# Performance work log

Measured on AMD Instinct MI355X. Metric: run time of the kernel, lower is better.

Reference implementation:

```python
import jax, jax.numpy as jnp
import numpy as np

# ----- constants derived from SNNNetwork.__init__ kwargs -----
T, B = 500, 32                     # steps = sim_time/dt = 25/0.05
ARCH = [512, 1024, 512]
DT = 0.05
R = 1.0 / 9.43
I0 = 700.0
K_M = 1.0 / (R * I0 * DT)          # as in __init__: k_m = 1/(R*I0*dt)
THRESH = 10.0                      # fixed plausible threshold (torch code derives it from `target`, but is non-runnable)
SPIKE_R = 20.0
SIGMA_V = 10.0
V_RESET = 0.0
ASC_AMP = np.array([-9.18, -198.94], np.float32)
ASC_R = np.array([1.0, 1.0], np.float32)
ASC_K = np.array([0.003, 0.1], np.float32)


def setup_inputs() -> dict:
    key = jax.random.key(0)
    k1, k2, k3 = jax.random.split(key, 3)
    inputs = jax.random.normal(k1, (T, B, ARCH[0]), dtype=jnp.float32)
    # nn.init.uniform_(linear.weight, wt-1, wt+1); use small symmetric range
    W1 = jax.random.uniform(k2, (ARCH[1], ARCH[0]), jnp.float32, -0.05, 0.05)
    W2 = jax.random.uniform(k3, (ARCH[2], ARCH[1]), jnp.float32, -0.05, 0.05)
    return {"inputs": inputs, "W1": W1, "W2": W2}


def _neuron_step(state, x):
    """One GLIFR (rate-based GLIF with after-spike currents) update.
    state = (v [B,N], asc [2,B,N]); x is synaptic drive [B,N].
    Returns (new_state, spikes [B,N]).
    """
    v, asc = state
    amp = jnp.asarray(ASC_AMP)[:, None, None]
    rmul = jnp.asarray(ASC_R)[:, None, None]
    kasc = jnp.asarray(ASC_K)[:, None, None]
    syn = I0 * x                                          # k_syn = 1
    i_total = syn + asc.sum(0)
    s = SPIKE_R * jax.nn.sigmoid((v - THRESH) / SIGMA_V)  # smooth spike rate
    s_dt = s * DT
    asc_new = asc * (1.0 - DT * kasc) + s_dt * (rmul * asc + amp)
    v_new = v + DT * K_M * (R * i_total - (v - V_RESET)) + s_dt * (V_RESET - v)
    return (v_new, asc_new), s


def reference(inputs, W1, W2):
    Bc = inputs.shape[1]

    def zstate(n):
        return (jnp.zeros((Bc, n), inputs.dtype), jnp.zeros((2, Bc, n), inputs.dtype))

    init = (zstate(ARCH[0]), jnp.zeros((Bc, ARCH[0]), inputs.dtype),
            zstate(ARCH[1]), jnp.zeros((Bc, ARCH[1]), inputs.dtype),
            zstate(ARCH[2]))

    def step(carry, x):
        st0, buf0, st1, buf1, st2 = carry
        # layer 0: no linear, raw input drives the neuron
        st0, s0 = _neuron_step(st0, x)
        # layer 1: delayed (delay=1) spikes of layer 0 through Linear
        st1, s1 = _neuron_step(st1, buf0 @ W1.T)
        # layer 2: delayed spikes of layer 1 through Linear
        st2, s2 = _neuron_step(st2, buf1 @ W2.T)
        return (st0, s0, st1, s1, st2), s2

    _, spikes_all = jax.lax.scan(step, init, inputs)
    return spikes_all  # [T, B, ARCH[-1]] == layers[-1].spikes_all
```

## Files before the change

kernel.cpp:

```cpp
#include <hip/hip_runtime.h>
#include <hip/hip_bf16.h>
#include <stdint.h>

#define TSTEPS 500
#define BB 32
#define N0 512
#define N1 1024
#define N2 512

typedef unsigned short ushort_t;
typedef __attribute__((ext_vector_type(8))) short short8;
typedef __attribute__((ext_vector_type(4))) float f32x4;

__device__ __forceinline__ ushort_t f2b(float x) {
    union { float f; uint32_t u; } c; c.f = x;
    uint32_t r = (c.u + 0x7fffu + ((c.u >> 16) & 1u)) >> 16;
    return (ushort_t)r;
}
__device__ __forceinline__ float b2f(ushort_t u) {
    union { uint32_t u; float f; } c; c.u = ((uint32_t)u) << 16;
    return c.f;
}

__device__ __forceinline__ float glifr_step(float& v, float& a0, float& a1,
                                            float x) {
    const float INV_I0 = 1.0f / 700.0f;
    const float C2 = 9.43f / 700.0f;
    const float CE = 0.14426950408889634f;
    const float CE10 = 1.4426950408889634f;
    const float C0 = 1.0f - 0.05f * 0.003f;
    const float C1 = 1.0f - 0.05f * 0.1f;
    const float AMP0 = -9.18f, AMP1 = -198.94f;

    float asum = a0 + a1;
    float drv = fmaf(asum, INV_I0, x);
    float e = exp2f(fmaf(v, -CE, CE10));
    float sig = __builtin_amdgcn_rcpf(1.0f + e);
    float na0 = fmaf(sig, a0 + AMP0, a0 * C0);
    float na1 = fmaf(sig, a1 + AMP1, a1 * C1);
    float nv = fmaf(-sig, v, fmaf(-C2, v, v + drv));
    a0 = na0; a1 = na1; v = nv;
    return sig;
}

#define PD 20
template <int NW, int MODE>
__global__ void scan_kernel(const float* __restrict__ drive,
                            float* __restrict__ sout) {
    const int idx = blockIdx.x * blockDim.x + threadIdx.x;
    const int S = BB * NW;

    auto LD = [&](int t) -> float {
        if (MODE == 0) return drive[(size_t)t * S + idx];
        return (t == 0) ? 0.0f : drive[(size_t)(t - 1) * S + idx];
    };

    float v = 0.f, a0 = 0.f, a1 = 0.f;

    auto STEP = [&](int t, float x) {
        float sig = glifr_step(v, a0, a1, x);
        sout[(size_t)t * S + idx] = (MODE == 2) ? 20.0f * sig : sig;
    };

    float p[PD];
#pragma unroll
    for (int i = 0; i < PD; ++i) p[i] = LD(i);

    for (int t = 0; t < TSTEPS - PD; t += PD) {
        float q[PD];
#pragma unroll
        for (int i = 0; i < PD; ++i) q[i] = LD(t + PD + i);
#pragma unroll
        for (int i = 0; i < PD; ++i) STEP(t + i, p[i]);
#pragma unroll
        for (int i = 0; i < PD; ++i) p[i] = q[i];
    }
#pragma unroll
    for (int i = 0; i < PD; ++i) STEP(TSTEPS - PD + i, p[i]);
}

__global__ void wsplit(const float* __restrict__ W1, const float* __restrict__ W2,
                       ushort_t* __restrict__ w1h, ushort_t* __restrict__ w1l,
                       ushort_t* __restrict__ w2h, ushort_t* __restrict__ w2l) {
    int i = blockIdx.x * 256 + threadIdx.x;
    float a = 20.0f * W1[i];
    ushort_t h = f2b(a);
    w1h[i] = h; w1l[i] = f2b(a - b2f(h));
    float b = 20.0f * W2[i];
    h = f2b(b);
    w2h[i] = h; w2l[i] = f2b(b - b2f(h));
}

template <int NBY>
__global__ __launch_bounds__(256, 2) void gemm_x3(
    const float* __restrict__ A,
    const ushort_t* __restrict__ Bh, const ushort_t* __restrict__ Bl,
    float* __restrict__ C, int Ncols, int K) {
    __shared__ char lds[32768];
    const int tid = threadIdx.x;
    const int lane = tid & 63, wave = tid >> 6;

    const int id = blockIdx.x, nwg = gridDim.x;
    const int qq = nwg >> 3, rr = nwg & 7;
    const int xcd = id & 7, jj = id >> 3;
    const int wg = (xcd < rr ? xcd * (qq + 1) : rr * (qq + 1) + (xcd - rr) * qq) + jj;
    const int m0 = (wg / NBY) * 128;
    const int n0 = (wg % NBY) * 128;

    const ushort_t* gB = (wave == 2) ? Bh : Bl;
    const int chunk_sw = (lane & 3) ^ ((lane >> 3) & 3);
    const size_t rowbB = (size_t)K * 2;
    const char* gsrcB = (const char*)gB +
                        (size_t)(n0 + (lane >> 2)) * rowbB + (size_t)chunk_sw * 16;

    const int r0 = tid >> 3, c4 = tid & 7;
    const int ch = (c4 >> 1) ^ ((r0 >> 1) & 3);
    const int aoff = r0 * 64 + ch * 16 + (c4 & 1) * 8;
    const float* aSrc = A + (size_t)(m0 + r0) * K + c4 * 4;

    const int KSTEPS = K / 32;
    f32x4 acc[4][4];
#pragma unroll
    for (int i = 0; i < 4; ++i)
#pragma unroll
        for (int j = 0; j < 4; ++j) acc[i][j] = (f32x4){0.f, 0.f, 0.f, 0.f};

    const int wm = wave >> 1, wn = wave & 1;
    const int r4 = lane & 15, kg = lane >> 4;
    const int slot = kg ^ ((r4 >> 1) & 3);
    const int fA = (wm * 64 + r4) * 64 + slot * 16;
    const int fB = (wn * 64 + r4) * 64 + slot * 16;

    for (int ks = 0; ks < KSTEPS; ++ks) {
        if (wave >= 2) {
#pragma unroll
            for (int i = 0; i < 8; ++i) {
                __builtin_amdgcn_global_load_lds(
                    (const __attribute__((address_space(1))) uint32_t*)(
                        gsrcB + (size_t)i * 16 * rowbB + (size_t)ks * 64),
                    (__attribute__((address_space(3))) uint32_t*)(
                        lds + 16384 + (wave - 2) * 8192 + i * 1024),
                    16, 0, 0);
            }
        }
#pragma unroll
        for (int i = 0; i < 4; ++i) {
            const float4 av = *reinterpret_cast<const float4*>(
                aSrc + (size_t)i * 32 * K + (size_t)ks * 32);
            __hip_bfloat162 h01 = __float22bfloat162_rn(make_float2(av.x, av.y));
            __hip_bfloat162 h23 = __float22bfloat162_rn(make_float2(av.z, av.w));
            uint32_t hi01 = *reinterpret_cast<uint32_t*>(&h01);
            uint32_t hi23 = *reinterpret_cast<uint32_t*>(&h23);
            float lx = av.x - __uint_as_float(hi01 << 16);
            float ly = av.y - __uint_as_float(hi01 & 0xffff0000u);
            float lz = av.z - __uint_as_float(hi23 << 16);
            float lw = av.w - __uint_as_float(hi23 & 0xffff0000u);
            __hip_bfloat162 l01 = __float22bfloat162_rn(make_float2(lx, ly));
            __hip_bfloat162 l23 = __float22bfloat162_rn(make_float2(lz, lw));
            uint32_t lo01 = *reinterpret_cast<uint32_t*>(&l01);
            uint32_t lo23 = *reinterpret_cast<uint32_t*>(&l23);
            *reinterpret_cast<uint2*>(lds + aoff + i * 2048) =
                make_uint2(hi01, hi23);
            *reinterpret_cast<uint2*>(lds + 8192 + aoff + i * 2048) =
                make_uint2(lo01, lo23);
        }
        __syncthreads();

        short8 ah[4], al[4], bh[4], bl[4];
#pragma unroll
        for (int i = 0; i < 4; ++i) {
            ah[i] = *(const short8*)(lds + 0     + fA + i * 1024);
            al[i] = *(const short8*)(lds + 8192  + fA + i * 1024);
            bh[i] = *(const short8*)(lds + 16384 + fB + i * 1024);
            bl[i] = *(const short8*)(lds + 24576 + fB + i * 1024);
        }
#pragma unroll
        for (int i = 0; i < 4; ++i)
#pragma unroll
            for (int j = 0; j < 4; ++j) {
                acc[i][j] = __builtin_amdgcn_mfma_f32_16x16x32_bf16(
                    ah[i], bh[j], acc[i][j], 0, 0, 0);
                acc[i][j] = __builtin_amdgcn_mfma_f32_16x16x32_bf16(
                    ah[i], bl[j], acc[i][j], 0, 0, 0);
                acc[i][j] = __builtin_amdgcn_mfma_f32_16x16x32_bf16(
                    al[i], bh[j], acc[i][j], 0, 0, 0);
            }
        __syncthreads();
    }

#pragma unroll
    for (int i = 0; i < 4; ++i)
#pragma unroll
        for (int j = 0; j < 4; ++j)
#pragma unroll
            for (int r = 0; r < 4; ++r) {
                int row = m0 + wm * 64 + i * 16 + kg * 4 + r;
                int col = n0 + wn * 64 + j * 16 + r4;
                C[(size_t)row * Ncols + col] = acc[i][j][r];
            }
}

extern "C" void kernel_launch(void* const* d_in, const int* in_sizes, int n_in,
                              void* d_out, int out_size, void* d_ws,
                              size_t ws_size, hipStream_t stream) {
    const float* inputs = (const float*)d_in[0];
    const float* W1 = (const float*)d_in[1];
    const float* W2 = (const float*)d_in[2];
    float* out = (float*)d_out;
    char* ws = (char*)d_ws;

    float* s0 = (float*)ws;
    float* s1 = (float*)ws;
    float* x1 = (float*)(ws + 65536000);
    float* x2 = (float*)(ws + 65536000);
    ushort_t* w1h = (ushort_t*)(ws + 131072000);
    ushort_t* w1l = (ushort_t*)(ws + 132120576);
    ushort_t* w2h = (ushort_t*)(ws + 133169152);
    ushort_t* w2l = (ushort_t*)(ws + 134217728);

    wsplit<<<2048, 256, 0, stream>>>(W1, W2, w1h, w1l, w2h, w2l);
    scan_kernel<N0, 0><<<256, 64, 0, stream>>>(inputs, s0);
    gemm_x3<8><<<1000, 256, 0, stream>>>(s0, w1h, w1l, x1, N1, N0);
    scan_kernel<N1, 1><<<512, 64, 0, stream>>>(x1, s1);
    gemm_x3<4><<<500, 256, 0, stream>>>(s1, w2h, w2l, x2, N2, N1);
    scan_kernel<N2, 2><<<256, 64, 0, stream>>>(x2, out);
}
```

Baseline: 219.5 us.

## Double-buffer GEMM LDS, pre-split spikes into packed bf16 pairs, fuse weight split

The scan kernels now write each spike rate as a packed hi/lo bf16 pair, so the GEMM only permutes bytes instead of converting fp32 per k-step. The GEMM uses two LDS buffers (64KB) so global loads for the next k-step overlap MFMA compute on the current one. The weight split kernel is merged into the first scan launch as extra blocks, saving a launch. Doubling LDS may reduce occupancy below the two blocks per CU the launch bounds request.

```diff
diff --git a/kernel.cpp b/kernel.cpp
--- a/kernel.cpp
+++ b/kernel.cpp
@@ -45,9 +45,9 @@
 
 #define PD 20
 template <int NW, int MODE>
-__global__ void scan_kernel(const float* __restrict__ drive,
-                            float* __restrict__ sout) {
-    const int idx = blockIdx.x * blockDim.x + threadIdx.x;
+__device__ __forceinline__ void scan_body(const float* __restrict__ drive,
+                                          uint32_t* __restrict__ pout,
+                                          float* __restrict__ fout, int idx) {
     const int S = BB * NW;
 
     auto LD = [&](int t) -> float {
@@ -59,7 +59,14 @@
 
     auto STEP = [&](int t, float x) {
         float sig = glifr_step(v, a0, a1, x);
-        sout[(size_t)t * S + idx] = (MODE == 2) ? 20.0f * sig : sig;
+        size_t o = (size_t)t * S + idx;
+        if (MODE == 2) {
+            fout[o] = 20.0f * sig;
+        } else {
+            ushort_t hi = f2b(sig);
+            float lo = sig - b2f(hi);
+            pout[o] = (uint32_t)hi | ((uint32_t)f2b(lo) << 16);
+        }
     };
 
     float p[PD];
@@ -79,24 +86,45 @@
     for (int i = 0; i < PD; ++i) STEP(TSTEPS - PD + i, p[i]);
 }
 
-__global__ void wsplit(const float* __restrict__ W1, const float* __restrict__ W2,
-                       ushort_t* __restrict__ w1h, ushort_t* __restrict__ w1l,
-                       ushort_t* __restrict__ w2h, ushort_t* __restrict__ w2l) {
-    int i = blockIdx.x * 256 + threadIdx.x;
-    float a = 20.0f * W1[i];
-    ushort_t h = f2b(a);
-    w1h[i] = h; w1l[i] = f2b(a - b2f(h));
-    float b = 20.0f * W2[i];
-    h = f2b(b);
-    w2h[i] = h; w2l[i] = f2b(b - b2f(h));
+__global__ void scan0_wsplit(const float* __restrict__ inputs,
+                             uint32_t* __restrict__ s0,
+                             const float* __restrict__ W1,
+                             const float* __restrict__ W2,
+                             ushort_t* __restrict__ w1h, ushort_t* __restrict__ w1l,
+                             ushort_t* __restrict__ w2h, ushort_t* __restrict__ w2l) {
+    const int bid = blockIdx.x;
+    if (bid < (BB * N0) / 64) {
+        scan_body<N0, 0>(inputs, s0, nullptr, bid * 64 + threadIdx.x);
+    } else {
+        int i = (bid - (BB * N0) / 64) * 64 + threadIdx.x;
+        float a = 20.0f * W1[i];
+        ushort_t h = f2b(a);
+        w1h[i] = h; w1l[i] = f2b(a - b2f(h));
+        float b = 20.0f * W2[i];
+        h = f2b(b);
+        w2h[i] = h; w2l[i] = f2b(b - b2f(h));
+    }
+}
+
+template <int NW>
+__global__ void scan_mid(const float* __restrict__ drive,
+                         uint32_t* __restrict__ sout) {
+    scan_body<NW, 1>(drive, sout, nullptr,
+                     blockIdx.x * blockDim.x + threadIdx.x);
+}
+
+__global__ void scan_last(const float* __restrict__ drive,
+                          float* __restrict__ out) {
+    scan_body<N2, 2>(drive, nullptr, out,
+                     blockIdx.x * blockDim.x + threadIdx.x);
 }
 
 template <int NBY>
 __global__ __launch_bounds__(256, 2) void gemm_x3(
-    const float* __restrict__ A,
+    const uint32_t* __restrict__ Apk,
     const ushort_t* __restrict__ Bh, const ushort_t* __restrict__ Bl,
     float* __restrict__ C, int Ncols, int K) {
-    __shared__ char lds[32768];
+    __shared__ char lds[65536];
     const int tid = threadIdx.x;
     const int lane = tid & 63, wave = tid >> 6;
 
@@ -116,9 +144,10 @@
     const int r0 = tid >> 3, c4 = tid & 7;
     const int ch = (c4 >> 1) ^ ((r0 >> 1) & 3);
     const int aoff = r0 * 64 + ch * 16 + (c4 & 1) * 8;
-    const float* aSrc = A + (size_t)(m0 + r0) * K + c4 * 4;
+    const uint32_t* aSrc = Apk + (size_t)(m0 + r0) * K + c4 * 4;
 
     const int KSTEPS = K / 32;
+
     f32x4 acc[4][4];
 #pragma unroll
     for (int i = 0; i < 4; ++i)
@@ -131,48 +160,44 @@
     const int fA = (wm * 64 + r4) * 64 + slot * 16;
     const int fB = (wn * 64 + r4) * 64 + slot * 16;
 
-    for (int ks = 0; ks < KSTEPS; ++ks) {
-        if (wave >= 2) {
-#pragma unroll
-            for (int i = 0; i < 8; ++i) {
-                __builtin_amdgcn_global_load_lds(
-                    (const __attribute__((address_space(1))) uint32_t*)(
-                        gsrcB + (size_t)i * 16 * rowbB + (size_t)ks * 64),
-                    (__attribute__((address_space(3))) uint32_t*)(
-                        lds + 16384 + (wave - 2) * 8192 + i * 1024),
-                    16, 0, 0);
-            }
-        }
+    auto issueB = [&](int ks, int base) {
+#pragma unroll
+        for (int i = 0; i < 8; ++i) {
+            __builtin_amdgcn_global_load_lds(
+                (const __attribute__((address_space(1))) uint32_t*)(
+                    gsrcB + (size_t)i * 16 * rowbB + (size_t)ks * 64),
+                (__attribute__((address_space(3))) uint32_t*)(
+                    lds + base + 16384 + (wave - 2) * 8192 + i * 1024),
+                16, 0, 0);
+        }
+    };
+    auto loadA = [&](int ks, uint4* pk) {
+#pragma unroll
+        for (int i = 0; i < 4; ++i)
+            pk[i] = *reinterpret_cast<const uint4*>(
+                aSrc + (size_t)i * 32 * K + (size_t)ks * 32);
+    };
+    auto writeA = [&](const uint4* pk, int base) {
 #pragma unroll
         for (int i = 0; i < 4; ++i) {
-            const float4 av = *reinterpret_cast<const float4*>(
-                aSrc + (size_t)i * 32 * K + (size_t)ks * 32);
-            __hip_bfloat162 h01 = __float22bfloat162_rn(make_float2(av.x, av.y));
-            __hip_bfloat162 h23 = __float22bfloat162_rn(make_float2(av.z, av.w));
-            uint32_t hi01 = *reinterpret_cast<uint32_t*>(&h01);
-            uint32_t hi23 = *reinterpret_cast<uint32_t*>(&h23);
-            float lx = av.x - __uint_as_float(hi01 << 16);
-            float ly = av.y - __uint_as_float(hi01 & 0xffff0000u);
-            float lz = av.z - __uint_as_float(hi23 << 16);
-            float lw = av.w - __uint_as_float(hi23 & 0xffff0000u);
-            __hip_bfloat162 l01 = __float22bfloat162_rn(make_float2(lx, ly));
-            __hip_bfloat162 l23 = __float22bfloat162_rn(make_float2(lz, lw));
-            uint32_t lo01 = *reinterpret_cast<uint32_t*>(&l01);
-            uint32_t lo23 = *reinterpret_cast<uint32_t*>(&l23);
-            *reinterpret_cast<uint2*>(lds + aoff + i * 2048) =
+            uint32_t hi01 = __builtin_amdgcn_perm(pk[i].y, pk[i].x, 0x05040100u);
+            uint32_t lo01 = __builtin_amdgcn_perm(pk[i].y, pk[i].x, 0x07060302u);
+            uint32_t hi23 = __builtin_amdgcn_perm(pk[i].w, pk[i].z, 0x05040100u);
+            uint32_t lo23 = __builtin_amdgcn_perm(pk[i].w, pk[i].z, 0x07060302u);
+            *reinterpret_cast<uint2*>(lds + base + aoff + i * 2048) =
                 make_uint2(hi01, hi23);
-            *reinterpret_cast<uint2*>(lds + 8192 + aoff + i * 2048) =
+            *reinterpret_cast<uint2*>(lds + base + 8192 + aoff + i * 2048) =
                 make_uint2(lo01, lo23);
         }
-        __syncthreads();
-
+    };
+    auto compute = [&](int base) {
         short8 ah[4], al[4], bh[4], bl[4];
 #pragma unroll
         for (int i = 0; i < 4; ++i) {
-            ah[i] = *(const short8*)(lds + 0     + fA + i * 1024);
-            al[i] = *(const short8*)(lds + 8192  + fA + i * 1024);
-            bh[i] = *(const short8*)(lds + 16384 + fB + i * 1024);
-            bl[i] = *(const short8*)(lds + 24576 + fB + i * 1024);
+            ah[i] = *(const short8*)(lds + base + 0     + fA + i * 1024);
+            al[i] = *(const short8*)(lds + base + 8192  + fA + i * 1024);
+            bh[i] = *(const short8*)(lds + base + 16384 + fB + i * 1024);
+            bl[i] = *(const short8*)(lds + base + 24576 + fB + i * 1024);
         }
 #pragma unroll
         for (int i = 0; i < 4; ++i)
@@ -185,7 +210,34 @@
                 acc[i][j] = __builtin_amdgcn_mfma_f32_16x16x32_bf16(
                     al[i], bh[j], acc[i][j], 0, 0, 0);
             }
+    };
+
+    {
+        if (wave >= 2) issueB(0, 0);
+        uint4 pk[4];
+        loadA(0, pk);
+        writeA(pk, 0);
         __syncthreads();
+    }
+
+    for (int ks = 0; ks < KSTEPS; ks += 2) {
+        {
+            if (wave >= 2) issueB(ks + 1, 32768);
+            uint4 pk[4];
+            loadA(ks + 1, pk);
+            compute(0);
+            writeA(pk, 32768);
+            __syncthreads();
+        }
+        {
+            const bool more = (ks + 2 < KSTEPS);
+            uint4 pk[4];
+            if (wave >= 2 && more) issueB(ks + 2, 0);
+            if (more) loadA(ks + 2, pk);
+            compute(32768);
+            if (more) writeA(pk, 0);
+            __syncthreads();
+        }
     }
 
 #pragma unroll
@@ -209,19 +261,19 @@
     float* out = (float*)d_out;
     char* ws = (char*)d_ws;
 
-    float* s0 = (float*)ws;
-    float* s1 = (float*)ws;
-    float* x1 = (float*)(ws + 65536000);
-    float* x2 = (float*)(ws + 65536000);
+    uint32_t* s0 = (uint32_t*)ws;
+    uint32_t* s1 = (uint32_t*)ws;
+    float*    x1 = (float*)(ws + 65536000);
+    float*    x2 = (float*)(ws + 65536000);
     ushort_t* w1h = (ushort_t*)(ws + 131072000);
     ushort_t* w1l = (ushort_t*)(ws + 132120576);
     ushort_t* w2h = (ushort_t*)(ws + 133169152);
     ushort_t* w2l = (ushort_t*)(ws + 134217728);
 
-    wsplit<<<2048, 256, 0, stream>>>(W1, W2, w1h, w1l, w2h, w2l);
-    scan_kernel<N0, 0><<<256, 64, 0, stream>>>(inputs, s0);
+    scan0_wsplit<<<256 + 8192, 64, 0, stream>>>(inputs, s0, W1, W2,
+                                                w1h, w1l, w2h, w2l);
     gemm_x3<8><<<1000, 256, 0, stream>>>(s0, w1h, w1l, x1, N1, N0);
-    scan_kernel<N1, 1><<<512, 64, 0, stream>>>(x1, s1);
+    scan_mid<N1><<<512, 64, 0, stream>>>(x1, s1);
     gemm_x3<4><<<500, 256, 0, stream>>>(s1, w2h, w2l, x2, N2, N1);
-    scan_kernel<N2, 2><<<256, 64, 0, stream>>>(x2, out);
-}
+    scan_last<<<256, 64, 0, stream>>>(x2, out);
+}
```

New measurement: 211.7 us. 3.5% less time.
